# Performance work log

Hardware: AMD Instinct MI355X
Metric: run time of the kernel (lower is better)

Reference implementation:

```python
import jax, jax.numpy as jnp
import numpy as np

N_NODES = 100000
N_EDGES = 1600000
N_GRAPHS = 64
BN_EPS = 1e-5


def setup_inputs() -> dict:
    key = jax.random.key(0)
    ks = jax.random.split(key, 16)
    inp = {
        'x': jax.random.normal(ks[0], (N_NODES, 768), dtype=jnp.float32),
        'edge_index': jax.random.randint(ks[1], (2, N_EDGES), 0, N_NODES, dtype=jnp.int32),
        'batch': jnp.sort(jax.random.randint(ks[2], (N_NODES,), 0, N_GRAPHS, dtype=jnp.int32)),
        'W_in': jax.random.normal(ks[3], (768, 256), dtype=jnp.float32) * 0.02,
        'b_in': jax.random.normal(ks[4], (256,), dtype=jnp.float32) * 0.02,
        'W_g': jax.random.normal(ks[5], (3, 256, 256), dtype=jnp.float32) * 0.05,
        'b_g': jax.random.normal(ks[6], (3, 256), dtype=jnp.float32) * 0.02,
        'bn_gamma': jax.random.uniform(ks[7], (3, 256), dtype=jnp.float32) + 0.5,
        'bn_beta': jax.random.normal(ks[8], (3, 256), dtype=jnp.float32) * 0.02,
        'bn_mean': jax.random.normal(ks[9], (3, 256), dtype=jnp.float32) * 0.02,
        'bn_var': jax.random.uniform(ks[10], (3, 256), dtype=jnp.float32) + 0.5,
        'W1': jax.random.normal(ks[11], (256, 128), dtype=jnp.float32) * 0.06,
        'b1': jax.random.normal(ks[12], (128,), dtype=jnp.float32) * 0.02,
        'W2': jax.random.normal(ks[13], (128, 128), dtype=jnp.float32) * 0.08,
        'b2': jax.random.normal(ks[14], (128,), dtype=jnp.float32) * 0.02,
    }
    return inp


def reference(x, edge_index, batch, W_in, b_in, W_g, b_g, bn_gamma, bn_beta,
              bn_mean, bn_var, W1, b1, W2, b2):
    N = x.shape[0]
    # Add self loops (PyG GCNConv default)
    loop = jnp.arange(N, dtype=edge_index.dtype)
    src = jnp.concatenate([edge_index[0], loop])  # [E+N]
    dst = jnp.concatenate([edge_index[1], loop])
    # Symmetric GCN normalization: deg over dst after self loops
    deg = jax.ops.segment_sum(jnp.ones_like(src, dtype=x.dtype), dst, num_segments=N)
    dinv = jnp.where(deg > 0, jax.lax.rsqrt(deg), 0.0)
    norm = (dinv[src] * dinv[dst])[:, None]  # [E+N, 1]

    # input projection + relu
    h = jax.nn.relu(x @ W_in + b_in)  # [N, 256]

    for i in range(W_g.shape[0]):
        m = h @ W_g[i]                                   # [N, 256]
        agg = jax.ops.segment_sum(m[src] * norm, dst, num_segments=N) + b_g[i]
        # BatchNorm (eval mode, running stats)
        agg = (agg - bn_mean[i]) * (bn_gamma[i] * jax.lax.rsqrt(bn_var[i] + BN_EPS)) + bn_beta[i]
        h = jax.nn.relu(agg)  # dropout is identity in eval

    # global mean pool per graph
    sums = jax.ops.segment_sum(h, batch, num_segments=N_GRAPHS)       # [G, 256]
    cnts = jax.ops.segment_sum(jnp.ones((N,), x.dtype), batch, num_segments=N_GRAPHS)
    g = sums / jnp.maximum(cnts, 1.0)[:, None]

    # output MLP
    out = jax.nn.relu(g @ W1 + b1) @ W2 + b2  # [G, 128]
    return out
```

## Files before the change

kernel.cpp:

```cpp
#include <hip/hip_runtime.h>
#include <hip/hip_fp16.h>

#define HIDDEN 256

using bfrag = __attribute__((ext_vector_type(8))) short;
using facc16 = __attribute__((ext_vector_type(16))) float;

#define BARRIER_LGKM()                                   \
  do {                                                   \
    asm volatile("s_waitcnt lgkmcnt(0)" ::: "memory");   \
    __builtin_amdgcn_s_barrier();                        \
  } while (0)

__device__ inline short bf16_rne(float x) {
  unsigned u = __builtin_bit_cast(unsigned, x);
  unsigned r = u + 0x7FFFu + ((u >> 16) & 1u);
  return (short)(r >> 16);
}
__device__ inline float bf16_to_f(short h) {
  unsigned u = ((unsigned)(unsigned short)h) << 16;
  return __builtin_bit_cast(float, u);
}
__device__ inline float h2f(unsigned short h) {
  return __half2float(__builtin_bit_cast(__half, h));
}
__device__ inline void cvt8(const float4& a, const float4& b, bfrag& hi, bfrag& lo) {
  float av[8] = {a.x, a.y, a.z, a.w, b.x, b.y, b.z, b.w};
#pragma unroll
  for (int i = 0; i < 8; ++i) {
    unsigned u = __builtin_bit_cast(unsigned, av[i]);
    hi[i] = (short)(u >> 16);
    float r = av[i] - __builtin_bit_cast(float, u & 0xFFFF0000u);
    lo[i] = (short)(__builtin_bit_cast(unsigned, r) >> 16);
  }
}

__global__ __launch_bounds__(256) void k_hist(const int* __restrict__ dst,
                                              int* __restrict__ deg, int E) {
  for (int e = blockIdx.x * blockDim.x + threadIdx.x; e < E;
       e += gridDim.x * blockDim.x)
    atomicAdd(&deg[dst[e]], 1);
}

__global__ __launch_bounds__(256) void k_scan_a(const int* __restrict__ deg,
                                                int* __restrict__ bsum, int N) {
  const int t = threadIdx.x, lane = t & 63, w = t >> 6;
  const int idx = blockIdx.x * 256 + t;
  int x = (idx < N) ? deg[idx] : 0;
#pragma unroll
  for (int off = 32; off >= 1; off >>= 1) x += __shfl_xor(x, off);
  __shared__ int ws[4];
  if (lane == 0) ws[w] = x;
  __syncthreads();
  if (t == 0) bsum[blockIdx.x] = ws[0] + ws[1] + ws[2] + ws[3];
}

__global__ __launch_bounds__(512) void k_scan_b(const int* __restrict__ bsum,
                                                int* __restrict__ boff, int nb) {
  const int t = threadIdx.x, lane = t & 63, w = t >> 6;
  int orig = (t < nb) ? bsum[t] : 0;
  int x = orig;
#pragma unroll
  for (int off = 1; off < 64; off <<= 1) {
    int y = __shfl_up(x, off);
    if (lane >= off) x += y;
  }
  __shared__ int wsum[8];
  if (lane == 63) wsum[w] = x;
  __syncthreads();
  if (w == 0 && lane < 8) {
    int s = wsum[lane];
#pragma unroll
    for (int off = 1; off < 8; off <<= 1) {
      int y = __shfl_up(s, off);
      if (lane >= off) s += y;
    }
    wsum[lane] = s;
  }
  __syncthreads();
  int inc = x + (w > 0 ? wsum[w - 1] : 0);
  if (t < nb) boff[t] = inc - orig;
}

__global__ __launch_bounds__(256) void k_scan_c(const int* __restrict__ deg,
                                                const int* __restrict__ boff,
                                                int* __restrict__ row_ptr,
                                                float* __restrict__ dinv, int N) {
  const int t = threadIdx.x, lane = t & 63, w = t >> 6;
  const int idx = blockIdx.x * 256 + t;
  int d = (idx < N) ? deg[idx] : 0;
  int x = d;
#pragma unroll
  for (int off = 1; off < 64; off <<= 1) {
    int y = __shfl_up(x, off);
    if (lane >= off) x += y;
  }
  __shared__ int ws[4];
  if (lane == 63) ws[w] = x;
  __syncthreads();
  int add = boff[blockIdx.x];
#pragma unroll
  for (int j = 0; j < 4; ++j)
    if (j < w) add += ws[j];
  if (idx < N) {
    row_ptr[idx + 1] = x + add;
    dinv[idx] = 1.0f / sqrtf((float)d + 1.0f);
  }
  if (idx == 0) row_ptr[0] = 0;
}

__global__ __launch_bounds__(256) void k_fill(const int* __restrict__ src,
                                              const int* __restrict__ dst,
                                              const int* __restrict__ row_ptr,
                                              int* __restrict__ fill,
                                              int* __restrict__ csr, int E) {
  for (int e = blockIdx.x * blockDim.x + threadIdx.x; e < E;
       e += gridDim.x * blockDim.x) {
    int d = dst[e];
    int pos = atomicAdd(&fill[d], 1);
    csr[row_ptr[d] + pos] = src[e];
  }
}

__global__ __launch_bounds__(256) void k_prep_w(const float* __restrict__ W_in,
                                                const float* __restrict__ W_g,
                                                short* __restrict__ Wt) {
  const int e = blockIdx.x * blockDim.x + threadIdx.x;
  if (e >= 196608 + 3 * 65536) return;
  float v;
  int k, n;
  size_t base;
  if (e < 196608) {
    k = e >> 8;
    n = e & 255;
    v = W_in[e];
    base = 0;
  } else {
    int r = e - 196608;
    int lyr = r >> 16;
    k = (r >> 8) & 255;
    n = r & 255;
    v = W_g[r];
    base = 393216 + (size_t)lyr * 131072;
  }
  size_t pos = base + (size_t)(k >> 5) * 16384 + (size_t)n * 32 + (k & 31);
  short hi = bf16_rne(v);
  short lo = bf16_rne(v - bf16_to_f(hi));
  Wt[pos] = hi;
  Wt[pos + 8192] = lo;
}

template <int EPI>
__global__ __launch_bounds__(256, 3) void gemm_mfma(const float* __restrict__ A,
                                                    const short* __restrict__ Wt,
                                                    const float* __restrict__ aux,
                                                    float* __restrict__ C,
                                                    int M, int K) {
  __shared__ short As[2][64][66];
  const int t = threadIdx.x;
  const int w = t >> 6, l = t & 63;
  const int g2 = l >> 5, l31 = l & 31;
  const int row0 = blockIdx.x * 64;
  const int colbase = w * 64;
  const int arow = t >> 2, ak = (t & 3) << 3;

  facc16 acc[2][2];
#pragma unroll
  for (int i = 0; i < 2; ++i)
#pragma unroll
    for (int j = 0; j < 2; ++j) acc[i][j] = (facc16)(0.0f);

  const int nsteps = K >> 5;
  const int ga = row0 + arow;
  const bool aval = ga < M;
  const float* aptr = A + (size_t)ga * K + ak;

  float4 f0 = make_float4(0.f, 0.f, 0.f, 0.f), f1 = f0;
  if (aval) {
    f0 = *(const float4*)aptr;
    f1 = *(const float4*)(aptr + 4);
  }
  {
    bfrag hi, lo;
    cvt8(f0, f1, hi, lo);
    *(bfrag*)&As[0][arow][ak] = hi;
    *(bfrag*)&As[0][arow][32 + ak] = lo;
  }
  if (nsteps > 1 && aval) {
    f0 = *(const float4*)(aptr + 32);
    f1 = *(const float4*)(aptr + 36);
  }

  int cur = 0;
  for (int s = 0; s < nsteps; ++s) {
    BARRIER_LGKM();
    bfrag bh[2][2], bl[2][2];
#pragma unroll
    for (int nt = 0; nt < 2; ++nt)
#pragma unroll
      for (int kh = 0; kh < 2; ++kh) {
        const short* wbp = Wt + ((size_t)s << 14) +
                           (size_t)(colbase + nt * 32 + l31) * 32 + kh * 16 + g2 * 8;
        bh[nt][kh] = *(const bfrag*)wbp;
        bl[nt][kh] = *(const bfrag*)(wbp + 8192);
      }
#pragma unroll
    for (int kh = 0; kh < 2; ++kh) {
      bfrag ah[2], al[2];
#pragma unroll
      for (int mt = 0; mt < 2; ++mt) {
        ah[mt] = *(const bfrag*)&As[cur][mt * 32 + l31][kh * 16 + g2 * 8];
        al[mt] = *(const bfrag*)&As[cur][mt * 32 + l31][32 + kh * 16 + g2 * 8];
      }
#pragma unroll
      for (int mt = 0; mt < 2; ++mt)
#pragma unroll
        for (int nt = 0; nt < 2; ++nt)
          acc[mt][nt] = __builtin_amdgcn_mfma_f32_32x32x16_bf16(
              ah[mt], bh[nt][kh], acc[mt][nt], 0, 0, 0);
#pragma unroll
      for (int mt = 0; mt < 2; ++mt)
#pragma unroll
        for (int nt = 0; nt < 2; ++nt)
          acc[mt][nt] = __builtin_amdgcn_mfma_f32_32x32x16_bf16(
              ah[mt], bl[nt][kh], acc[mt][nt], 0, 0, 0);
#pragma unroll
      for (int mt = 0; mt < 2; ++mt)
#pragma unroll
        for (int nt = 0; nt < 2; ++nt)
          acc[mt][nt] = __builtin_amdgcn_mfma_f32_32x32x16_bf16(
              al[mt], bh[nt][kh], acc[mt][nt], 0, 0, 0);
    }
    if (s + 1 < nsteps) {
      bfrag hi, lo;
      cvt8(f0, f1, hi, lo);
      *(bfrag*)&As[cur ^ 1][arow][ak] = hi;
      *(bfrag*)&As[cur ^ 1][arow][32 + ak] = lo;
      if (s + 2 < nsteps && aval) {
        const float* ap = aptr + (size_t)(s + 2) * 32;
        f0 = *(const float4*)ap;
        f1 = *(const float4*)(ap + 4);
      }
    }
    cur ^= 1;
  }
  if (EPI == 0) {
#pragma unroll
    for (int nt = 0; nt < 2; ++nt) {
      const int col = colbase + nt * 32 + l31;
      const float bias = aux[col];
#pragma unroll
      for (int mt = 0; mt < 2; ++mt)
#pragma unroll
        for (int r = 0; r < 16; ++r) {
          int row = row0 + mt * 32 + (r & 3) + 8 * (r >> 2) + 4 * g2;
          if (row < M)
            C[(size_t)row * HIDDEN + col] = fmaxf(acc[mt][nt][r] + bias, 0.f);
        }
    }
  } else {
    __half* Ch = (__half*)C;
#pragma unroll
    for (int mt = 0; mt < 2; ++mt)
#pragma unroll
      for (int r = 0; r < 16; ++r) {
        int row = row0 + mt * 32 + (r & 3) + 8 * (r >> 2) + 4 * g2;
        if (row >= M) continue;
        const float sc = aux[row];
#pragma unroll
        for (int nt = 0; nt < 2; ++nt)
          Ch[(size_t)row * HIDDEN + colbase + nt * 32 + l31] =
              __float2half(acc[mt][nt][r] * sc);
      }
  }
}

__global__ __launch_bounds__(256) void k_aggregate(
    const unsigned short* __restrict__ mp, const int* __restrict__ row_ptr,
    const int* __restrict__ csr, const float* __restrict__ dinv,
    const float* __restrict__ bg, const float* __restrict__ gamma,
    const float* __restrict__ beta, const float* __restrict__ mean,
    const float* __restrict__ var, float* __restrict__ hout, int N) {
  const int wave = threadIdx.x >> 6, l = threadIdx.x & 63;
  const int v = blockIdx.x * 4 + wave;
  if (v >= N) return;
  const int co = l << 2;
  ushort4 rs = *(const ushort4*)(mp + (size_t)v * HIDDEN + co);
  float4 acc;
  acc.x = h2f(rs.x); acc.y = h2f(rs.y); acc.z = h2f(rs.z); acc.w = h2f(rs.w);
  const int s = row_ptr[v], e = row_ptr[v + 1];
  int i = s;
  for (; i + 8 <= e; i += 8) {
    ushort4 r0 = *(const ushort4*)(mp + (size_t)csr[i + 0] * HIDDEN + co);
    ushort4 r1 = *(const ushort4*)(mp + (size_t)csr[i + 1] * HIDDEN + co);
    ushort4 r2 = *(const ushort4*)(mp + (size_t)csr[i + 2] * HIDDEN + co);
    ushort4 r3 = *(const ushort4*)(mp + (size_t)csr[i + 3] * HIDDEN + co);
    ushort4 r4 = *(const ushort4*)(mp + (size_t)csr[i + 4] * HIDDEN + co);
    ushort4 r5 = *(const ushort4*)(mp + (size_t)csr[i + 5] * HIDDEN + co);
    ushort4 r6 = *(const ushort4*)(mp + (size_t)csr[i + 6] * HIDDEN + co);
    ushort4 r7 = *(const ushort4*)(mp + (size_t)csr[i + 7] * HIDDEN + co);
    acc.x += h2f(r0.x) + h2f(r1.x) + h2f(r2.x) + h2f(r3.x) +
             h2f(r4.x) + h2f(r5.x) + h2f(r6.x) + h2f(r7.x);
    acc.y += h2f(r0.y) + h2f(r1.y) + h2f(r2.y) + h2f(r3.y) +
             h2f(r4.y) + h2f(r5.y) + h2f(r6.y) + h2f(r7.y);
    acc.z += h2f(r0.z) + h2f(r1.z) + h2f(r2.z) + h2f(r3.z) +
             h2f(r4.z) + h2f(r5.z) + h2f(r6.z) + h2f(r7.z);
    acc.w += h2f(r0.w) + h2f(r1.w) + h2f(r2.w) + h2f(r3.w) +
             h2f(r4.w) + h2f(r5.w) + h2f(r6.w) + h2f(r7.w);
  }
  for (; i < e; ++i) {
    ushort4 r0 = *(const ushort4*)(mp + (size_t)csr[i] * HIDDEN + co);
    acc.x += h2f(r0.x);
    acc.y += h2f(r0.y);
    acc.z += h2f(r0.z);
    acc.w += h2f(r0.w);
  }
  const float dv = dinv[v];
  float4 bg4 = *(const float4*)&bg[co];
  float4 g4 = *(const float4*)&gamma[co];
  float4 be4 = *(const float4*)&beta[co];
  float4 mn4 = *(const float4*)&mean[co];
  float4 vr4 = *(const float4*)&var[co];
  float4 o;
  o.x = fmaxf((acc.x * dv + bg4.x - mn4.x) * (g4.x / sqrtf(vr4.x + 1e-5f)) + be4.x, 0.f);
  o.y = fmaxf((acc.y * dv + bg4.y - mn4.y) * (g4.y / sqrtf(vr4.y + 1e-5f)) + be4.y, 0.f);
  o.z = fmaxf((acc.z * dv + bg4.z - mn4.z) * (g4.z / sqrtf(vr4.z + 1e-5f)) + be4.z, 0.f);
  o.w = fmaxf((acc.w * dv + bg4.w - mn4.w) * (g4.w / sqrtf(vr4.w + 1e-5f)) + be4.w, 0.f);
  ((float4*)hout)[(size_t)v * 64 + l] = o;
}

__global__ __launch_bounds__(64) void k_count(const int* __restrict__ batch,
                                              float* __restrict__ cnt, int N,
                                              int G) {
  const int g = threadIdx.x;
  if (g >= G) return;
  int lo = 0, hi = N;
  while (lo < hi) {
    int mid = (lo + hi) >> 1;
    if (batch[mid] < g) lo = mid + 1; else hi = mid;
  }
  int lo2 = lo, hi2 = N;
  while (lo2 < hi2) {
    int mid = (lo2 + hi2) >> 1;
    if (batch[mid] < g + 1) lo2 = mid + 1; else hi2 = mid;
  }
  cnt[g] = (float)(lo2 - lo);
}

__global__ __launch_bounds__(256) void k_pool(const float* __restrict__ h,
                                              const int* __restrict__ batch,
                                              float* __restrict__ sums, int N) {
  const int t = threadIdx.x;
  const int start = blockIdx.x * 256;
  if (start >= N) return;
  const int end = min(start + 256, N);
  float acc = 0.f;
  int cur = batch[start];
  for (int n = start; n < end; ++n) {
    int g = batch[n];
    if (g != cur) {
      atomicAdd(&sums[cur * HIDDEN + t], acc);
      acc = 0.f;
      cur = g;
    }
    acc += h[(size_t)n * HIDDEN + t];
  }
  atomicAdd(&sums[cur * HIDDEN + t], acc);
}

__global__ __launch_bounds__(128) void k_head(const float* __restrict__ sums,
                                              const float* __restrict__ cnt,
                                              const float* __restrict__ W1,
                                              const float* __restrict__ b1,
                                              const float* __restrict__ W2,
                                              const float* __restrict__ b2,
                                              float* __restrict__ out) {
  __shared__ float gr[256];
  __shared__ float t1[128];
  const int b = blockIdx.x, t = threadIdx.x;
  const float inv = 1.0f / fmaxf(cnt[b], 1.0f);
  gr[t] = sums[b * HIDDEN + t] * inv;
  gr[t + 128] = sums[b * HIDDEN + t + 128] * inv;
  __syncthreads();
  float a = b1[t];
  for (int k = 0; k < 256; ++k) a += gr[k] * W1[k * 128 + t];
  t1[t] = fmaxf(a, 0.f);
  __syncthreads();
  float o = b2[t];
  for (int k = 0; k < 128; ++k) o += t1[k] * W2[k * 128 + t];
  out[b * 128 + t] = o;
}

extern "C" void kernel_launch(void* const* d_in, const int* in_sizes, int n_in,
                              void* d_out, int out_size, void* d_ws,
                              size_t ws_size, hipStream_t stream) {
  (void)n_in;
  (void)ws_size;
  const float* x = (const float*)d_in[0];
  const int* ei = (const int*)d_in[1];
  const int* batch = (const int*)d_in[2];
  const float* W_in = (const float*)d_in[3];
  const float* b_in = (const float*)d_in[4];
  const float* W_g = (const float*)d_in[5];
  const float* b_g = (const float*)d_in[6];
  const float* bn_gamma = (const float*)d_in[7];
  const float* bn_beta = (const float*)d_in[8];
  const float* bn_mean = (const float*)d_in[9];
  const float* bn_var = (const float*)d_in[10];
  const float* W1 = (const float*)d_in[11];
  const float* b1 = (const float*)d_in[12];
  const float* W2 = (const float*)d_in[13];
  const float* b2 = (const float*)d_in[14];

  const int KIN = 768;
  const int N = in_sizes[0] / KIN;
  const int E = in_sizes[1] / 2;
  const int G = out_size / 128;

  const int* src = ei;
  const int* dst = ei + E;

  char* ws = (char*)d_ws;
  size_t off = 0;
  auto take = [&](size_t bytes) -> void* {
    void* p = ws + off;
    off += (bytes + 255) & ~(size_t)255;
    return p;
  };
  float* h0 = (float*)take((size_t)N * HIDDEN * 4);
  unsigned short* h1 = (unsigned short*)take((size_t)N * HIDDEN * 2);
  float* dinv = (float*)take((size_t)N * 4);
  int* deg = (int*)take((size_t)N * 4);
  int* fill = (int*)take((size_t)N * 4);
  int* row_ptr = (int*)take((size_t)(N + 1) * 4);
  int* csr = (int*)take((size_t)E * 4);
  float* sums = (float*)take((size_t)G * HIDDEN * 4);
  float* cnt = (float*)take((size_t)G * 4);
  short* Wt = (short*)take((size_t)(393216 + 3 * 131072) * 2);
  const int nb = (N + 255) / 256;
  int* bsum = (int*)take((size_t)nb * 4);
  int* boff = (int*)take((size_t)nb * 4);

  hipMemsetAsync(deg, 0, (size_t)N * 4, stream);
  hipMemsetAsync(fill, 0, (size_t)N * 4, stream);
  hipMemsetAsync(sums, 0, (size_t)G * HIDDEN * 4, stream);

  k_prep_w<<<(196608 + 3 * 65536 + 255) / 256, 256, 0, stream>>>(W_in, W_g, Wt);
  k_hist<<<2048, 256, 0, stream>>>(dst, deg, E);
  k_scan_a<<<nb, 256, 0, stream>>>(deg, bsum, N);
  k_scan_b<<<1, 512, 0, stream>>>(bsum, boff, nb);
  k_scan_c<<<nb, 256, 0, stream>>>(deg, boff, row_ptr, dinv, N);
  k_fill<<<2048, 256, 0, stream>>>(src, dst, row_ptr, fill, csr, E);

  const int gx = (N + 63) / 64;
  gemm_mfma<0><<<gx, 256, 0, stream>>>(x, Wt, b_in, h0, N, KIN);
  for (int i = 0; i < 3; ++i) {
    gemm_mfma<1><<<gx, 256, 0, stream>>>(h0, Wt + 393216 + (size_t)i * 131072,
                                         dinv, (float*)h1, N, HIDDEN);
    k_aggregate<<<(N + 3) / 4, 256, 0, stream>>>(
        h1, row_ptr, csr, dinv, b_g + i * HIDDEN, bn_gamma + i * HIDDEN,
        bn_beta + i * HIDDEN, bn_mean + i * HIDDEN, bn_var + i * HIDDEN, h0, N);
  }
  k_count<<<1, 64, 0, stream>>>(batch, cnt, N, G);
  k_pool<<<(N + 255) / 256, 256, 0, stream>>>(h0, batch, sums, N);
  k_head<<<G, 128, 0, stream>>>(sums, cnt, W1, b1, W2, b2, (float*)d_out);
}
```

Baseline: 1.030 ms.

## Store activations in fp16, use f16 MFMA layer GEMMs, fuse graph-prep into GEMM launches

Hidden activations h0 are now stored as fp16 instead of fp32, which halves the traffic for the aggregate, pool and layer GEMM reads. The layer GEMMs use a new LDS-free f16 MFMA kernel, with weights split into hi/lo fp16 parts and register double-buffered loads. The degree histogram runs in the same launch as the input projection, and the CSR fill runs in the same launch as the first layer GEMM, so the graph-prep work overlaps GEMM work and a few launches are removed. The cost is reduced activation precision (fp16 rounding) and a larger register footprint in the new GEMM kernel.

```diff
diff --git a/kernel.cpp b/kernel.cpp
--- a/kernel.cpp
+++ b/kernel.cpp
@@ -4,6 +4,7 @@
 #define HIDDEN 256
 
 using bfrag = __attribute__((ext_vector_type(8))) short;
+using hfrag = __attribute__((ext_vector_type(8))) _Float16;
 using facc16 = __attribute__((ext_vector_type(16))) float;
 
 #define BARRIER_LGKM()                                   \
@@ -24,6 +25,9 @@
 __device__ inline float h2f(unsigned short h) {
   return __half2float(__builtin_bit_cast(__half, h));
 }
+__device__ inline unsigned short f2h_bits(float v) {
+  return __builtin_bit_cast(unsigned short, __float2half(v));
+}
 __device__ inline void cvt8(const float4& a, const float4& b, bfrag& hi, bfrag& lo) {
   float av[8] = {a.x, a.y, a.z, a.w, b.x, b.y, b.z, b.w};
 #pragma unroll
@@ -33,13 +37,6 @@
     float r = av[i] - __builtin_bit_cast(float, u & 0xFFFF0000u);
     lo[i] = (short)(__builtin_bit_cast(unsigned, r) >> 16);
   }
-}
-
-__global__ __launch_bounds__(256) void k_hist(const int* __restrict__ dst,
-                                              int* __restrict__ deg, int E) {
-  for (int e = blockIdx.x * blockDim.x + threadIdx.x; e < E;
-       e += gridDim.x * blockDim.x)
-    atomicAdd(&deg[dst[e]], 1);
 }
 
 __global__ __launch_bounds__(256) void k_scan_a(const int* __restrict__ deg,
@@ -109,19 +106,6 @@
   if (idx == 0) row_ptr[0] = 0;
 }
 
-__global__ __launch_bounds__(256) void k_fill(const int* __restrict__ src,
-                                              const int* __restrict__ dst,
-                                              const int* __restrict__ row_ptr,
-                                              int* __restrict__ fill,
-                                              int* __restrict__ csr, int E) {
-  for (int e = blockIdx.x * blockDim.x + threadIdx.x; e < E;
-       e += gridDim.x * blockDim.x) {
-    int d = dst[e];
-    int pos = atomicAdd(&fill[d], 1);
-    csr[row_ptr[d] + pos] = src[e];
-  }
-}
-
 __global__ __launch_bounds__(256) void k_prep_w(const float* __restrict__ W_in,
                                                 const float* __restrict__ W_g,
                                                 short* __restrict__ Wt) {
@@ -130,11 +114,13 @@
   float v;
   int k, n;
   size_t base;
+  bool isproj;
   if (e < 196608) {
     k = e >> 8;
     n = e & 255;
     v = W_in[e];
     base = 0;
+    isproj = true;
   } else {
     int r = e - 196608;
     int lyr = r >> 16;
@@ -142,25 +128,32 @@
     n = r & 255;
     v = W_g[r];
     base = 393216 + (size_t)lyr * 131072;
+    isproj = false;
   }
   size_t pos = base + (size_t)(k >> 5) * 16384 + (size_t)n * 32 + (k & 31);
-  short hi = bf16_rne(v);
-  short lo = bf16_rne(v - bf16_to_f(hi));
-  Wt[pos] = hi;
-  Wt[pos + 8192] = lo;
-}
-
-template <int EPI>
-__global__ __launch_bounds__(256, 3) void gemm_mfma(const float* __restrict__ A,
-                                                    const short* __restrict__ Wt,
-                                                    const float* __restrict__ aux,
-                                                    float* __restrict__ C,
-                                                    int M, int K) {
+  if (isproj) {
+    short hi = bf16_rne(v);
+    short lo = bf16_rne(v - bf16_to_f(hi));
+    Wt[pos] = hi;
+    Wt[pos + 8192] = lo;
+  } else {
+    __half hh = __float2half(v);
+    float r = v - __half2float(hh);
+    Wt[pos] = (short)__builtin_bit_cast(unsigned short, hh);
+    Wt[pos + 8192] = (short)__builtin_bit_cast(unsigned short, __float2half(r));
+  }
+}
+
+__device__ __forceinline__ void proj_body(int bx, const float* __restrict__ A,
+                                          const short* __restrict__ Wt,
+                                          const float* __restrict__ bias,
+                                          unsigned short* __restrict__ Ch,
+                                          int M, int K) {
   __shared__ short As[2][64][66];
   const int t = threadIdx.x;
   const int w = t >> 6, l = t & 63;
   const int g2 = l >> 5, l31 = l & 31;
-  const int row0 = blockIdx.x * 64;
+  const int row0 = bx * 64;
   const int colbase = w * 64;
   const int arow = t >> 2, ak = (t & 3) << 3;
 
@@ -244,35 +237,133 @@
     }
     cur ^= 1;
   }
-  if (EPI == 0) {
-#pragma unroll
-    for (int nt = 0; nt < 2; ++nt) {
-      const int col = colbase + nt * 32 + l31;
-      const float bias = aux[col];
-#pragma unroll
-      for (int mt = 0; mt < 2; ++mt)
-#pragma unroll
-        for (int r = 0; r < 16; ++r) {
-          int row = row0 + mt * 32 + (r & 3) + 8 * (r >> 2) + 4 * g2;
-          if (row < M)
-            C[(size_t)row * HIDDEN + col] = fmaxf(acc[mt][nt][r] + bias, 0.f);
-        }
-    }
-  } else {
-    __half* Ch = (__half*)C;
+#pragma unroll
+  for (int nt = 0; nt < 2; ++nt) {
+    const int col = colbase + nt * 32 + l31;
+    const float b = bias[col];
 #pragma unroll
     for (int mt = 0; mt < 2; ++mt)
 #pragma unroll
       for (int r = 0; r < 16; ++r) {
         int row = row0 + mt * 32 + (r & 3) + 8 * (r >> 2) + 4 * g2;
-        if (row >= M) continue;
-        const float sc = aux[row];
-#pragma unroll
-        for (int nt = 0; nt < 2; ++nt)
-          Ch[(size_t)row * HIDDEN + colbase + nt * 32 + l31] =
-              __float2half(acc[mt][nt][r] * sc);
+        if (row < M)
+          Ch[(size_t)row * HIDDEN + col] = f2h_bits(fmaxf(acc[mt][nt][r] + b, 0.f));
       }
   }
+}
+
+#define LG_LOAD(S, AA, BH, BL)                                          \
+  {                                                                     \
+    AA[0][0] = *(const hfrag*)(ap0 + (S) * 32);                         \
+    AA[0][1] = *(const hfrag*)(ap0 + (S) * 32 + 16);                    \
+    AA[1][0] = *(const hfrag*)(ap1 + (S) * 32);                         \
+    AA[1][1] = *(const hfrag*)(ap1 + (S) * 32 + 16);                    \
+    const short* wp = wb + ((size_t)(S) << 14);                         \
+    BH[0][0] = *(const hfrag*)(wp);                                     \
+    BH[0][1] = *(const hfrag*)(wp + 16);                                \
+    BH[1][0] = *(const hfrag*)(wp + 1024);                              \
+    BH[1][1] = *(const hfrag*)(wp + 1024 + 16);                         \
+    BL[0][0] = *(const hfrag*)(wp + 8192);                              \
+    BL[0][1] = *(const hfrag*)(wp + 8192 + 16);                         \
+    BL[1][0] = *(const hfrag*)(wp + 8192 + 1024);                       \
+    BL[1][1] = *(const hfrag*)(wp + 8192 + 1024 + 16);                  \
+  }
+
+#define LG_COMPUTE(AA, BH, BL)                                          \
+  _Pragma("unroll") for (int kh = 0; kh < 2; ++kh) {                    \
+    _Pragma("unroll") for (int mt = 0; mt < 2; ++mt)                    \
+        _Pragma("unroll") for (int nt = 0; nt < 2; ++nt) acc[mt][nt] =  \
+        __builtin_amdgcn_mfma_f32_32x32x16_f16(AA[mt][kh], BH[nt][kh],  \
+                                               acc[mt][nt], 0, 0, 0);   \
+    _Pragma("unroll") for (int mt = 0; mt < 2; ++mt)                    \
+        _Pragma("unroll") for (int nt = 0; nt < 2; ++nt) acc[mt][nt] =  \
+        __builtin_amdgcn_mfma_f32_32x32x16_f16(AA[mt][kh], BL[nt][kh],  \
+                                               acc[mt][nt], 0, 0, 0);   \
+  }
+
+__device__ __forceinline__ void layer_gemm_body(
+    int bx, const unsigned short* __restrict__ A, const short* __restrict__ Wt,
+    const float* __restrict__ dinv, unsigned short* __restrict__ Cm, int M) {
+  const int t = threadIdx.x;
+  const int w = t >> 6, l = t & 63;
+  const int g2 = l >> 5, l31 = l & 31;
+  const int row0 = bx * 64;
+  const int colbase = w * 64;
+
+  facc16 acc[2][2];
+#pragma unroll
+  for (int i = 0; i < 2; ++i)
+#pragma unroll
+    for (int j = 0; j < 2; ++j) acc[i][j] = (facc16)(0.0f);
+
+  int r0 = row0 + l31, r1 = row0 + 32 + l31;
+  if (r0 >= M) r0 = M - 1;
+  if (r1 >= M) r1 = M - 1;
+  const unsigned short* ap0 = A + (size_t)r0 * HIDDEN + g2 * 8;
+  const unsigned short* ap1 = A + (size_t)r1 * HIDDEN + g2 * 8;
+  const short* wb = Wt + (size_t)(colbase + l31) * 32 + g2 * 8;
+
+  hfrag aA[2][2], bhA[2][2], blA[2][2];
+  hfrag aB[2][2], bhB[2][2], blB[2][2];
+
+  LG_LOAD(0, aA, bhA, blA);
+#pragma unroll
+  for (int s = 0; s < 8; s += 2) {
+    if (s + 1 < 8) LG_LOAD(s + 1, aB, bhB, blB);
+    LG_COMPUTE(aA, bhA, blA);
+    if (s + 2 < 8) LG_LOAD(s + 2, aA, bhA, blA);
+    LG_COMPUTE(aB, bhB, blB);
+  }
+#pragma unroll
+  for (int mt = 0; mt < 2; ++mt)
+#pragma unroll
+    for (int r = 0; r < 16; ++r) {
+      int row = row0 + mt * 32 + (r & 3) + 8 * (r >> 2) + 4 * g2;
+      if (row >= M) continue;
+      const float sc = dinv[row];
+#pragma unroll
+      for (int nt = 0; nt < 2; ++nt)
+        Cm[(size_t)row * HIDDEN + colbase + nt * 32 + l31] =
+            f2h_bits(acc[mt][nt][r] * sc);
+    }
+}
+
+__global__ __launch_bounds__(256, 3) void k_mega1(
+    const float* __restrict__ x, const short* __restrict__ Wt,
+    const float* __restrict__ b_in, unsigned short* __restrict__ h0, int M,
+    int K, const int* __restrict__ dst, int* __restrict__ deg, int E,
+    int ngemm, int nhist) {
+  if ((int)blockIdx.x < ngemm) {
+    proj_body(blockIdx.x, x, Wt, b_in, h0, M, K);
+  } else {
+    const int b = blockIdx.x - ngemm;
+    for (int e = b * 256 + threadIdx.x; e < E; e += nhist * 256)
+      atomicAdd(&deg[dst[e]], 1);
+  }
+}
+
+__global__ __launch_bounds__(256, 2) void k_mega2(
+    const unsigned short* __restrict__ h0, const short* __restrict__ WtL,
+    const float* __restrict__ dinv, unsigned short* __restrict__ h1, int M,
+    const int* __restrict__ src, const int* __restrict__ dst,
+    const int* __restrict__ row_ptr, int* __restrict__ fill,
+    int* __restrict__ csr, int E, int ngemm, int nfill) {
+  if ((int)blockIdx.x < ngemm) {
+    layer_gemm_body(blockIdx.x, h0, WtL, dinv, h1, M);
+  } else {
+    const int b = blockIdx.x - ngemm;
+    for (int e = b * 256 + threadIdx.x; e < E; e += nfill * 256) {
+      int d = dst[e];
+      int pos = atomicAdd(&fill[d], 1);
+      csr[row_ptr[d] + pos] = src[e];
+    }
+  }
+}
+
+__global__ __launch_bounds__(256, 2) void k_gemm_layer(
+    const unsigned short* __restrict__ h, const short* __restrict__ WtL,
+    const float* __restrict__ dinv, unsigned short* __restrict__ m, int M) {
+  layer_gemm_body(blockIdx.x, h, WtL, dinv, m, M);
 }
 
 __global__ __launch_bounds__(256) void k_aggregate(
@@ -280,7 +371,7 @@
     const int* __restrict__ csr, const float* __restrict__ dinv,
     const float* __restrict__ bg, const float* __restrict__ gamma,
     const float* __restrict__ beta, const float* __restrict__ mean,
-    const float* __restrict__ var, float* __restrict__ hout, int N) {
+    const float* __restrict__ var, unsigned short* __restrict__ hout, int N) {
   const int wave = threadIdx.x >> 6, l = threadIdx.x & 63;
   const int v = blockIdx.x * 4 + wave;
   if (v >= N) return;
@@ -321,12 +412,12 @@
   float4 be4 = *(const float4*)&beta[co];
   float4 mn4 = *(const float4*)&mean[co];
   float4 vr4 = *(const float4*)&var[co];
-  float4 o;
-  o.x = fmaxf((acc.x * dv + bg4.x - mn4.x) * (g4.x / sqrtf(vr4.x + 1e-5f)) + be4.x, 0.f);
-  o.y = fmaxf((acc.y * dv + bg4.y - mn4.y) * (g4.y / sqrtf(vr4.y + 1e-5f)) + be4.y, 0.f);
-  o.z = fmaxf((acc.z * dv + bg4.z - mn4.z) * (g4.z / sqrtf(vr4.z + 1e-5f)) + be4.z, 0.f);
-  o.w = fmaxf((acc.w * dv + bg4.w - mn4.w) * (g4.w / sqrtf(vr4.w + 1e-5f)) + be4.w, 0.f);
-  ((float4*)hout)[(size_t)v * 64 + l] = o;
+  ushort4 o;
+  o.x = f2h_bits(fmaxf((acc.x * dv + bg4.x - mn4.x) * (g4.x / sqrtf(vr4.x + 1e-5f)) + be4.x, 0.f));
+  o.y = f2h_bits(fmaxf((acc.y * dv + bg4.y - mn4.y) * (g4.y / sqrtf(vr4.y + 1e-5f)) + be4.y, 0.f));
+  o.z = f2h_bits(fmaxf((acc.z * dv + bg4.z - mn4.z) * (g4.z / sqrtf(vr4.z + 1e-5f)) + be4.z, 0.f));
+  o.w = f2h_bits(fmaxf((acc.w * dv + bg4.w - mn4.w) * (g4.w / sqrtf(vr4.w + 1e-5f)) + be4.w, 0.f));
+  *(ushort4*)&hout[(size_t)v * HIDDEN + co] = o;
 }
 
 __global__ __launch_bounds__(64) void k_count(const int* __restrict__ batch,
@@ -347,7 +438,7 @@
   cnt[g] = (float)(lo2 - lo);
 }
 
-__global__ __launch_bounds__(256) void k_pool(const float* __restrict__ h,
+__global__ __launch_bounds__(256) void k_pool(const unsigned short* __restrict__ h,
                                               const int* __restrict__ batch,
                                               float* __restrict__ sums, int N) {
   const int t = threadIdx.x;
@@ -363,7 +454,7 @@
       acc = 0.f;
       cur = g;
     }
-    acc += h[(size_t)n * HIDDEN + t];
+    acc += h2f(h[(size_t)n * HIDDEN + t]);
   }
   atomicAdd(&sums[cur * HIDDEN + t], acc);
 }
@@ -427,7 +518,7 @@
     off += (bytes + 255) & ~(size_t)255;
     return p;
   };
-  float* h0 = (float*)take((size_t)N * HIDDEN * 4);
+  unsigned short* h0 = (unsigned short*)take((size_t)N * HIDDEN * 2);
   unsigned short* h1 = (unsigned short*)take((size_t)N * HIDDEN * 2);
   float* dinv = (float*)take((size_t)N * 4);
   int* deg = (int*)take((size_t)N * 4);
@@ -445,18 +536,23 @@
   hipMemsetAsync(fill, 0, (size_t)N * 4, stream);
   hipMemsetAsync(sums, 0, (size_t)G * HIDDEN * 4, stream);
 
+  const int gx = (N + 63) / 64;
+  const int NH = 256;
+  const int NF = 256;
+
   k_prep_w<<<(196608 + 3 * 65536 + 255) / 256, 256, 0, stream>>>(W_in, W_g, Wt);
-  k_hist<<<2048, 256, 0, stream>>>(dst, deg, E);
+  k_mega1<<<gx + NH, 256, 0, stream>>>(x, Wt, b_in, h0, N, KIN, dst, deg, E,
+                                       gx, NH);
   k_scan_a<<<nb, 256, 0, stream>>>(deg, bsum, N);
   k_scan_b<<<1, 512, 0, stream>>>(bsum, boff, nb);
   k_scan_c<<<nb, 256, 0, stream>>>(deg, boff, row_ptr, dinv, N);
-  k_fill<<<2048, 256, 0, stream>>>(src, dst, row_ptr, fill, csr, E);
-
-  const int gx = (N + 63) / 64;
-  gemm_mfma<0><<<gx, 256, 0, stream>>>(x, Wt, b_in, h0, N, KIN);
-  for (int i = 0; i < 3; ++i) {
-    gemm_mfma<1><<<gx, 256, 0, stream>>>(h0, Wt + 393216 + (size_t)i * 131072,
-                                         dinv, (float*)h1, N, HIDDEN);
+  k_mega2<<<gx + NF, 256, 0, stream>>>(h0, Wt + 393216, dinv, h1, N, src, dst,
+                                       row_ptr, fill, csr, E, gx, NF);
+  k_aggregate<<<(N + 3) / 4, 256, 0, stream>>>(
+      h1, row_ptr, csr, dinv, b_g, bn_gamma, bn_beta, bn_mean, bn_var, h0, N);
+  for (int i = 1; i < 3; ++i) {
+    k_gemm_layer<<<gx, 256, 0, stream>>>(h0, Wt + 393216 + (size_t)i * 131072,
+                                         dinv, h1, N);
     k_aggregate<<<(N + 3) / 4, 256, 0, stream>>>(
         h1, row_ptr, csr, dinv, b_g + i * HIDDEN, bn_gamma + i * HIDDEN,
         bn_beta + i * HIDDEN, bn_mean + i * HIDDEN, bn_var + i * HIDDEN, h0, N);
```

Result: faster. 988.1 us (-4.1%).
